# Performance work log

Measured on AMD Instinct MI355X. Metric: run time of the kernel, lower is better.

## Reference

```python
import jax, jax.numpy as jnp
import numpy as np

HS = 512   # hidden_size
IN = 2048  # input_size
MB = 100   # memory_bank_size
T  = 4096  # nImg


def setup_inputs() -> dict:
    key = jax.random.key(0)
    ks = jax.random.split(key, 20)

    def w(k, i, o):
        return jax.random.normal(k, (i, o), jnp.float32) * (1.0 / np.sqrt(i))

    def b(k, o):
        return jax.random.normal(k, (o,), jnp.float32) * 0.01

    return {
        "hidden_out_a": jax.random.normal(ks[0], (T, IN), jnp.float32),
        "hidden_out_m": jax.random.normal(ks[1], (T, IN), jnp.float32),
        "W_ca": w(ks[2], HS + IN, HS),  "b_ca": b(ks[3], HS),    # hidden_to_content_a
        "W_cm": w(ks[4], HS + IN, HS),  "b_cm": b(ks[5], HS),    # hidden_to_content_m
        "W_wp": w(ks[6], 3 * HS, 3),    "b_wp": b(ks[7], 3),     # write_prob
        "W_wpa": w(ks[8], HS + IN, MB), "b_wpa": b(ks[9], MB),   # write_prob_a
        "W_wpm": w(ks[10], HS + IN, MB),"b_wpm": b(ks[11], MB),  # write_prob_m
        "W_rp": w(ks[12], 3 * HS, MB),  "b_rp": b(ks[13], MB),   # read_prob
        "W_rh": w(ks[14], 2 * HS, HS),  "b_rh": b(ks[15], HS),   # read_to_hidden
        "W_rha": w(ks[16], 2 * HS + IN, HS), "b_rha": b(ks[17], HS),  # read_to_hidden_a
        "W_rhm": w(ks[18], 2 * HS + IN, HS), "b_rhm": b(ks[19], HS),  # read_to_hidden_m
        "nImg": T,
    }


def reference(hidden_out_a, hidden_out_m,
              W_ca, b_ca, W_cm, b_cm,
              W_wp, b_wp, W_wpa, b_wpa, W_wpm, b_wpm,
              W_rp, b_rp, W_rh, b_rh,
              W_rha, b_rha, W_rhm, b_rhm,
              nImg):
    hs = W_rh.shape[1]
    mb = W_rp.shape[1]

    def step(carry, xs):
        mem, h, ha, hm = carry            # mem: [MB, HS]; h/ha/hm: [HS]
        xa, xm = xs                       # [IN] each
        xh = jnp.concatenate([ha, hm, h])               # [3*HS]
        ar = jax.nn.softmax(xh @ W_rp + b_rp)           # [MB]
        r = ar @ mem                                    # [HS] memory read
        h1 = jax.nn.relu(jnp.concatenate([r, h]) @ W_rh + b_rh)
        ha1 = jax.nn.relu(jnp.concatenate([xa, r, ha]) @ W_rha + b_rha)
        hm1 = jax.nn.relu(jnp.concatenate([xm, r, hm]) @ W_rhm + b_rhm)
        aw = jax.nn.softmax(xh @ W_wp + b_wp)           # [3] stream gate
        xha = jnp.concatenate([ha, xa])                 # [HS+IN]
        xhm = jnp.concatenate([hm, xm])
        c_a = jax.nn.relu(xha @ W_ca + b_ca)            # [HS]
        c_m = jax.nn.relu(xhm @ W_cm + b_cm)
        aw_a = jax.nn.softmax(xha @ W_wpa + b_wpa)      # [MB]
        aw_m = jax.nn.softmax(xhm @ W_wpm + b_wpm)
        mem = aw[0] * mem + aw[1] * aw_a[:, None] * c_a + aw[2] * aw_m[:, None] * c_m
        return (mem, h1, ha1, hm1), h1

    init = (jnp.zeros((mb, hs), hidden_out_a.dtype),
            jnp.zeros((hs,), hidden_out_a.dtype),
            jnp.zeros((hs,), hidden_out_a.dtype),
            jnp.zeros((hs,), hidden_out_a.dtype))
    _, hiddens = jax.lax.scan(step, init,
                              (hidden_out_a[:nImg], hidden_out_m[:nImg]))
    return hiddens  # [nImg, HS]
```

## Files before the change

kernel.cpp:

```cpp
#include <hip/hip_runtime.h>
#include <cstdint>
#include <cstddef>

#define HS 512

constexpr int TPB  = 512;
constexpr int GBLK = 64;
constexpr int OWNB = 24;
constexpr int OWNW = 3;

constexpr size_t OFF_TWrp  = 0;
constexpr size_t OFF_TWwp  = OFF_TWrp  + 100*1536;
constexpr size_t OFF_TWwpa = OFF_TWwp  + 3*1536;
constexpr size_t OFF_TWwpm = OFF_TWwpa + 100*512;
constexpr size_t OFF_TWca  = OFF_TWwpm + 100*512;
constexpr size_t OFF_TWcm  = OFF_TWca  + 512*512;
constexpr size_t OFF_TWh0  = OFF_TWcm  + 512*512;
constexpr size_t OFF_TWh1  = OFF_TWh0  + 512*512;
constexpr size_t OFF_TWh2  = OFF_TWh1  + 512*512;
constexpr size_t OFF_TWu0  = OFF_TWh2  + 512*512;
constexpr size_t OFF_TWu1  = OFF_TWu0  + 512*512;
constexpr size_t OFF_TWu2  = OFF_TWu1  + 512*512;
constexpr size_t OFF_PAca  = OFF_TWu2  + 512*512;
constexpr size_t OFF_PMcm  = OFF_PAca  + 4096*512;
constexpr size_t OFF_PArha = OFF_PMcm  + 4096*512;
constexpr size_t OFF_PMrhm = OFF_PArha + 4096*512;
constexpr size_t OFF_PAwpa = OFF_PMrhm + 4096*512;
constexpr size_t OFF_PMwpm = OFF_PAwpa + 4096*100;
constexpr size_t OFF_CARRY = OFF_PMwpm + 4096*100;
constexpr size_t OFF_BCAST = OFF_CARRY + 2*1536*2;

__device__ __forceinline__ unsigned long long ald(const unsigned long long* p) {
  return __hip_atomic_load(const_cast<unsigned long long*>(p),
                           __ATOMIC_RELAXED, __HIP_MEMORY_SCOPE_AGENT);
}
__device__ __forceinline__ void gstTag(unsigned long long* p, float v, unsigned tag) {
  unsigned long long u = ((unsigned long long)tag << 32) | (unsigned long long)__float_as_uint(v);
  __hip_atomic_store(p, u, __ATOMIC_RELAXED, __HIP_MEMORY_SCOPE_AGENT);
}
__device__ __forceinline__ float xrsum(float v) {
  #pragma unroll
  for (int o = 32; o; o >>= 1) v += __shfl_xor(v, o, 64);
  return v;
}

template<int K4>
__device__ __forceinline__ float dotK(const float* __restrict__ w, const float* x) {
  int l = threadIdx.x & 63;
  const float4* w4 = (const float4*)w;
  const float4* x4 = (const float4*)x;
  float acc = 0.f;
  #pragma unroll
  for (int it = 0; it < K4; ++it) {
    float4 a = w4[l + 64*it];
    float4 b = x4[l + 64*it];
    acc += a.x*b.x + a.y*b.y + a.z*b.z + a.w*b.w;
  }
  return acc;
}

__device__ __forceinline__ void dot2K512(const float* __restrict__ w,
                                         const float* xa, const float* xm,
                                         float& ra, float& rm) {
  int l = threadIdx.x & 63;
  const float4* w4 = (const float4*)w;
  const float4* a4 = (const float4*)xa;
  const float4* m4 = (const float4*)xm;
  float sa = 0.f, sm = 0.f;
  #pragma unroll
  for (int it = 0; it < 2; ++it) {
    float4 wv = w4[l + 64*it], av = a4[l + 64*it], mv = m4[l + 64*it];
    sa += wv.x*av.x + wv.y*av.y + wv.z*av.z + wv.w*av.w;
    sm += wv.x*mv.x + wv.y*mv.y + wv.z*mv.z + wv.w*mv.w;
  }
  #pragma unroll
  for (int o = 32; o; o >>= 1) { sa += __shfl_xor(sa, o, 64); sm += __shfl_xor(sm, o, 64); }
  ra = sa; rm = sm;
}

__global__ void initK(unsigned long long* carryT, unsigned long long* bcast) {
  int i = blockIdx.x * blockDim.x + threadIdx.x, st = gridDim.x * blockDim.x;
  for (int k = i; k < 1536; k += st) carryT[k] = (1ull << 32);
  for (int k = i; k < 1536; k += st) carryT[1536 + k] = 0ull;
  for (int k = i; k < 2 * 1344; k += st) bcast[k] = 0ull;
}

__global__ void transK(const float* __restrict__ src, float* __restrict__ dst, int R, int C) {
  __shared__ float tile[32][33];
  int c0 = blockIdx.x * 32, r0 = blockIdx.y * 32;
  for (int i = threadIdx.y; i < 32; i += 8) {
    int r = r0 + i, c = c0 + threadIdx.x;
    tile[i][threadIdx.x] = (r < R && c < C) ? src[(size_t)r * C + c] : 0.f;
  }
  __syncthreads();
  for (int i = threadIdx.y; i < 32; i += 8) {
    int c = c0 + i, r = r0 + threadIdx.x;
    if (c < C && r < R) dst[(size_t)c * R + r] = tile[threadIdx.x][i];
  }
}

__global__ __launch_bounds__(256) void gemmK(const float* __restrict__ X,
                                             const float* __restrict__ W,
                                             float* __restrict__ C, int N) {
  __shared__ float As[16][68];
  __shared__ float Bs[16][68];
  int t0 = blockIdx.y * 64, n0 = blockIdx.x * 64;
  int tid = threadIdx.x, tx = tid & 15, ty = tid >> 4;
  float acc[4][4] = {};
  for (int k0 = 0; k0 < 2048; k0 += 16) {
    {
      int r = tid >> 2, c = (tid & 3) * 4;
      float4 v = *(const float4*)(X + (size_t)(t0 + r) * 2048 + k0 + c);
      As[c + 0][r] = v.x; As[c + 1][r] = v.y; As[c + 2][r] = v.z; As[c + 3][r] = v.w;
    }
    {
      int kr = tid >> 4, c = (tid & 15) * 4;
      int gcol = n0 + c;
      const float* src = W + (size_t)(k0 + kr) * N + gcol;
      #pragma unroll
      for (int i = 0; i < 4; ++i) Bs[kr][c + i] = (gcol + i < N) ? src[i] : 0.f;
    }
    __syncthreads();
    #pragma unroll
    for (int kk = 0; kk < 16; ++kk) {
      float4 a4 = *(const float4*)&As[kk][ty * 4];
      float4 b4 = *(const float4*)&Bs[kk][tx * 4];
      float av[4] = {a4.x, a4.y, a4.z, a4.w};
      float bv[4] = {b4.x, b4.y, b4.z, b4.w};
      #pragma unroll
      for (int i = 0; i < 4; ++i)
        #pragma unroll
        for (int j = 0; j < 4; ++j) acc[i][j] += av[i] * bv[j];
    }
    __syncthreads();
  }
  #pragma unroll
  for (int i = 0; i < 4; ++i)
    #pragma unroll
    for (int j = 0; j < 4; ++j) {
      int col = n0 + tx * 4 + j;
      if (col < N) C[(size_t)(t0 + ty * 4 + i) * N + col] = acc[i][j];
    }
}

__global__ __launch_bounds__(256) void gemm128(const float* __restrict__ X,
                                               const float* __restrict__ W,
                                               float* __restrict__ C) {
  __shared__ float As[8][132];
  __shared__ float Bs[8][132];
  const int N = 512;
  int t0 = blockIdx.y * 128, n0 = blockIdx.x * 128;
  int tid = threadIdx.x, tx = tid & 15, ty = tid >> 4;
  float acc[8][8] = {};
  for (int k0 = 0; k0 < 2048; k0 += 8) {
    int r = tid >> 1, c4 = (tid & 1) * 4;
    float4 va = *(const float4*)(X + (size_t)(t0 + r) * 2048 + k0 + c4);
    int kr = tid >> 5, cb = (tid & 31) * 4;
    float4 vb = *(const float4*)(W + (size_t)(k0 + kr) * N + n0 + cb);
    __syncthreads();
    As[c4 + 0][r] = va.x; As[c4 + 1][r] = va.y; As[c4 + 2][r] = va.z; As[c4 + 3][r] = va.w;
    Bs[kr][cb] = vb.x; Bs[kr][cb + 1] = vb.y; Bs[kr][cb + 2] = vb.z; Bs[kr][cb + 3] = vb.w;
    __syncthreads();
    #pragma unroll
    for (int kk = 0; kk < 8; ++kk) {
      float av[8], bv[8];
      *(float4*)av       = *(const float4*)&As[kk][ty * 8];
      *(float4*)(av + 4) = *(const float4*)&As[kk][ty * 8 + 4];
      *(float4*)bv       = *(const float4*)&Bs[kk][tx * 8];
      *(float4*)(bv + 4) = *(const float4*)&Bs[kk][tx * 8 + 4];
      #pragma unroll
      for (int i = 0; i < 8; ++i)
        #pragma unroll
        for (int j = 0; j < 8; ++j) acc[i][j] += av[i] * bv[j];
    }
  }
  #pragma unroll
  for (int i = 0; i < 8; ++i) {
    float* dst = C + (size_t)(t0 + ty * 8 + i) * N + n0 + tx * 8;
    *(float4*)dst       = *(float4*)&acc[i][0];
    *(float4*)(dst + 4) = *(float4*)&acc[i][4];
  }
}

struct RArgs {
  const float *TWrp, *TWwp, *TWwpa, *TWwpm, *TWca, *TWcm;
  const float *TWh0, *TWh1, *TWh2, *TWu0, *TWu1, *TWu2;
  const float *PAca, *PMcm, *PArha, *PMrhm, *PAwpa, *PMwpm;
  const float *b_ca, *b_cm, *b_wp, *b_wpa, *b_wpm, *b_rp, *b_rh, *b_rha, *b_rhm;
  unsigned long long *carryT, *bcast;
  float *out;
  int nT;
};

__global__ __launch_bounds__(TPB, 1) void recurK(RArgs a) {
  const int tid  = threadIdx.x;
  const int lane = tid & 63;
  const int lw   = tid >> 6;
  const int b    = blockIdx.x;

  __shared__ __align__(16) float s_wca[8 * 512];
  __shared__ __align__(16) float s_wcm[8 * 512];
  __shared__ __align__(16) float s_wbig[2 * 1536];
  __shared__ __align__(16) float s_wsm[4 * 512];
  __shared__ __align__(16) float s_TWu[OWNB * 512];
  __shared__ float s_G[OWNB * 104];
  __shared__ __align__(16) float s_x[1536];
  __shared__ __align__(16) float s_c[1024];
  __shared__ float s_ar[104], s_awa[104], s_awm[104], s_aw[4];
  __shared__ float s_part[OWNB];

  const int r0a = (b + 51) & 63;
  const int r1m = (b + 25) & 63;
  const bool big1_grp = (b < 36);
  const bool big1_wp  = (b >= 40 && b <= 42);

  for (int i = tid; i < 8 * 512; i += TPB) {
    int row = i >> 9, col = i & 511;
    s_wca[i] = a.TWca[(size_t)(b * 8 + row) * 512 + col];
    s_wcm[i] = a.TWcm[(size_t)(b * 8 + row) * 512 + col];
  }
  for (int i = tid; i < 1536; i += TPB) {
    s_wbig[i] = a.TWrp[(size_t)b * 1536 + i];
    float v2 = 0.f;
    if (big1_grp)      v2 = a.TWrp[(size_t)(b + 64) * 1536 + i];
    else if (big1_wp)  v2 = a.TWwp[(size_t)(b - 40) * 1536 + i];
    s_wbig[1536 + i] = v2;
  }
  for (int i = tid; i < 512; i += TPB) {
    s_wsm[i]        = a.TWwpa[(size_t)r0a * 512 + i];
    s_wsm[512 + i]  = (r0a < 36) ? a.TWwpa[(size_t)(r0a + 64) * 512 + i] : 0.f;
    s_wsm[1024 + i] = a.TWwpm[(size_t)r1m * 512 + i];
    s_wsm[1536 + i] = (r1m < 36) ? a.TWwpm[(size_t)(r1m + 64) * 512 + i] : 0.f;
  }
  for (int i = tid; i < OWNB * 512; i += TPB) {
    int rr = i >> 9, col = i & 511;
    int q = b * OWNB + rr, hsel = q >> 9, j = q & 511;
    const float* src = (hsel == 0) ? a.TWu0 : (hsel == 1) ? a.TWu1 : a.TWu2;
    s_TWu[i] = src[(size_t)j * 512 + col];
  }
  for (int i = tid; i < OWNB * 104; i += TPB) s_G[i] = 0.f;

  const int cacol = b * 8 + lw;
  const float bCa = a.b_ca[cacol];
  const float bCm = a.b_cm[cacol];

  int gtype = 0, gslot = 0, gdst = 0, gxoff = 0;
  const float* gpre = nullptr;
  float gbias = 0.f;
  if (lw == 7)      { gtype = 1; gslot = 0; gdst = 1024 + b; gbias = a.b_rp[b]; }
  else if (lw == 6) {
    if (big1_grp)     { gtype = 1; gslot = 1; gdst = 1024 + b + 64; gbias = a.b_rp[b + 64]; }
    else if (big1_wp) { gtype = 1; gslot = 1; gdst = 1324 + (b - 40); gbias = a.b_wp[b - 40]; }
  }
  else if (lw == 5) { gtype = 2; gslot = 0; gdst = 1124 + r0a; gxoff = 0;
                      gpre = a.PAwpa + r0a; gbias = a.b_wpa[r0a]; }
  else if (lw == 4 && r0a < 36) { gtype = 2; gslot = 1; gdst = 1124 + r0a + 64; gxoff = 0;
                      gpre = a.PAwpa + r0a + 64; gbias = a.b_wpa[r0a + 64]; }
  else if (lw == 3) { gtype = 2; gslot = 2; gdst = 1224 + r1m; gxoff = 512;
                      gpre = a.PMwpm + r1m; gbias = a.b_wpm[r1m]; }
  else if (lw == 2 && r1m < 36) { gtype = 2; gslot = 3; gdst = 1224 + r1m + 64; gxoff = 512;
                      gpre = a.PMwpm + r1m + 64; gbias = a.b_wpm[r1m + 64]; }

  int ownHsel[OWNW], ownJ[OWNW], whX[OWNW];
  float ownBias[OWNW];
  const float* ownPre[OWNW];
  const float* whRow[OWNW];
  #pragma unroll
  for (int k = 0; k < OWNW; ++k) {
    int q = b * OWNB + lw * OWNW + k, hsel = q >> 9, j = q & 511;
    ownHsel[k] = hsel; ownJ[k] = j;
    if (hsel == 0)      { ownBias[k] = a.b_rh[j];  ownPre[k] = nullptr;
                          whRow[k] = a.TWh0 + (size_t)j * 512; whX[k] = 1024; }
    else if (hsel == 1) { ownBias[k] = a.b_rha[j]; ownPre[k] = a.PArha + j;
                          whRow[k] = a.TWh1 + (size_t)j * 512; whX[k] = 0; }
    else                { ownBias[k] = a.b_rhm[j]; ownPre[k] = a.PMrhm + j;
                          whRow[k] = a.TWh2 + (size_t)j * 512; whX[k] = 512; }
  }
  __syncthreads();

  for (int t = 0; t < a.nT; ++t) {
    const unsigned tagB = (unsigned)t + 1;
    unsigned long long* bc = a.bcast + (size_t)(t & 1) * 1344;

    float preCa = a.PAca[(size_t)t * 512 + cacol];
    float preCm = a.PMcm[(size_t)t * 512 + cacol];
    float preG  = (gtype == 2) ? gpre[(size_t)t * 100] : 0.f;
    float preO[OWNW];
    #pragma unroll
    for (int k = 0; k < OWNW; ++k)
      preO[k] = ownPre[k] ? ownPre[k][(size_t)t * 512] : 0.f;

    {
      const unsigned long long* cin = a.carryT + (size_t)(t & 1) * 1536;
      int i0 = tid, i1 = tid + 512, i2 = tid + 1024;
      unsigned long long v0 = ald(cin + i0), v1 = ald(cin + i1), v2 = ald(cin + i2);
      while (((unsigned)(v0 >> 32) < tagB) | ((unsigned)(v1 >> 32) < tagB) |
             ((unsigned)(v2 >> 32) < tagB)) {
        __builtin_amdgcn_s_sleep(1);
        v0 = ald(cin + i0); v1 = ald(cin + i1); v2 = ald(cin + i2);
      }
      s_x[i0] = __uint_as_float((unsigned)v0);
      s_x[i1] = __uint_as_float((unsigned)v1);
      s_x[i2] = __uint_as_float((unsigned)v2);
    }
    __syncthreads();

    if (gtype == 1) {
      float v = xrsum(dotK<6>(s_wbig + gslot * 1536, s_x));
      if (!lane) gstTag(bc + gdst, v + gbias, tagB);
    } else if (gtype == 2) {
      float v = xrsum(dotK<2>(s_wsm + gslot * 512, s_x + gxoff));
      if (!lane) gstTag(bc + gdst, v + gbias + preG, tagB);
    }
    {
      float v = xrsum(dotK<2>(s_wca + lw * 512, s_x));
      if (!lane) gstTag(bc + cacol, fmaxf(v + preCa + bCa, 0.f), tagB);
      v = xrsum(dotK<2>(s_wcm + lw * 512, s_x + 512));
      if (!lane) gstTag(bc + 512 + cacol, fmaxf(v + preCm + bCm, 0.f), tagB);
    }
    #pragma unroll
    for (int k = 0; k < OWNW; ++k) {
      float v = xrsum(dotK<2>(whRow[k], s_x + whX[k]));
      if (!lane) s_part[lw * OWNW + k] = v;
    }

    if (lw < 3) {
      int base = 1024 + lw * 100;
      const unsigned long long* p1 = bc + base + lane;
      bool two = lane < 36;
      unsigned long long v1 = ald(p1);
      unsigned long long v2 = two ? ald(p1 + 64) : ~0ull;
      while (((unsigned)(v1 >> 32) < tagB) | ((unsigned)(v2 >> 32) < tagB)) {
        __builtin_amdgcn_s_sleep(1);
        v1 = ald(p1); if (two) v2 = ald(p1 + 64);
      }
      float x1 = __uint_as_float((unsigned)v1);
      float x2 = two ? __uint_as_float((unsigned)v2) : -3.0e38f;
      float m = fmaxf(x1, x2);
      #pragma unroll
      for (int o = 32; o; o >>= 1) m = fmaxf(m, __shfl_xor(m, o, 64));
      float e1 = expf(x1 - m);
      float e2 = two ? expf(x2 - m) : 0.f;
      float ss = e1 + e2;
      #pragma unroll
      for (int o = 32; o; o >>= 1) ss += __shfl_xor(ss, o, 64);
      float inv = 1.f / ss;
      float* dst = (lw == 0) ? s_ar : (lw == 1) ? s_awa : s_awm;
      dst[lane] = e1 * inv;
      if (two) dst[64 + lane] = e2 * inv;
    } else if (lw == 3) {
      float x = -3.0e38f;
      if (lane < 3) {
        const unsigned long long* p = bc + 1324 + lane;
        unsigned long long v = ald(p);
        while ((unsigned)(v >> 32) < tagB) { __builtin_amdgcn_s_sleep(1); v = ald(p); }
        x = __uint_as_float((unsigned)v);
      }
      float m = x;
      #pragma unroll
      for (int o = 32; o; o >>= 1) m = fmaxf(m, __shfl_xor(m, o, 64));
      float e = (lane < 3) ? expf(x - m) : 0.f;
      float ss = e;
      #pragma unroll
      for (int o = 32; o; o >>= 1) ss += __shfl_xor(ss, o, 64);
      if (lane < 3) s_aw[lane] = e / ss;
    } else {
      int base = tid - 256;
      const unsigned long long* p = bc + base;
      unsigned long long v0 = ald(p), v1 = ald(p + 256), v2 = ald(p + 512), v3 = ald(p + 768);
      while (((unsigned)(v0 >> 32) < tagB) | ((unsigned)(v1 >> 32) < tagB) |
             ((unsigned)(v2 >> 32) < tagB) | ((unsigned)(v3 >> 32) < tagB)) {
        __builtin_amdgcn_s_sleep(1);
        v0 = ald(p); v1 = ald(p + 256); v2 = ald(p + 512); v3 = ald(p + 768);
      }
      s_c[base]       = __uint_as_float((unsigned)v0);
      s_c[base + 256] = __uint_as_float((unsigned)v1);
      s_c[base + 512] = __uint_as_float((unsigned)v2);
      s_c[base + 768] = __uint_as_float((unsigned)v3);
    }
    __syncthreads();

    const float aw0 = s_aw[0], aw1 = s_aw[1], aw2 = s_aw[2];
    unsigned long long* cout = a.carryT + (size_t)((t + 1) & 1) * 1536;
    #pragma unroll
    for (int k = 0; k < OWNW; ++k) {
      int rr = lw * OWNW + k;
      float uA, uM;
      dot2K512(s_TWu + (size_t)rr * 512, s_c, s_c + 512, uA, uM);

      float* grow = s_G + rr * 104;
      bool two = lane < 36;
      float g1 = grow[lane];
      float g2 = two ? grow[64 + lane] : 0.f;
      float contrib = s_ar[lane] * g1 + (two ? s_ar[64 + lane] * g2 : 0.f);
      contrib = xrsum(contrib);
      grow[lane] = aw0 * g1 + aw1 * s_awa[lane] * uA + aw2 * s_awm[lane] * uM;
      if (two)
        grow[64 + lane] = aw0 * g2 + aw1 * s_awa[64 + lane] * uA + aw2 * s_awm[64 + lane] * uM;

      if (!lane) {
        int j = ownJ[k];
        float h = fmaxf(contrib + s_part[rr] + preO[k] + ownBias[k], 0.f);
        if (ownHsel[k] == 0) {
          a.out[(size_t)t * 512 + j] = h;
          gstTag(cout + 1024 + j, h, tagB + 1);
        } else if (ownHsel[k] == 1) {
          gstTag(cout + j, h, tagB + 1);
        } else {
          gstTag(cout + 512 + j, h, tagB + 1);
        }
      }
    }
    __syncthreads();
  }
}

extern "C" void kernel_launch(void* const* d_in, const int* in_sizes, int n_in,
                              void* d_out, int out_size, void* d_ws, size_t ws_size,
                              hipStream_t stream) {
  const float* Xa    = (const float*)d_in[0];
  const float* Xm    = (const float*)d_in[1];
  const float* W_ca  = (const float*)d_in[2];  const float* b_ca  = (const float*)d_in[3];
  const float* W_cm  = (const float*)d_in[4];  const float* b_cm  = (const float*)d_in[5];
  const float* W_wp  = (const float*)d_in[6];  const float* b_wp  = (const float*)d_in[7];
  const float* W_wpa = (const float*)d_in[8];  const float* b_wpa = (const float*)d_in[9];
  const float* W_wpm = (const float*)d_in[10]; const float* b_wpm = (const float*)d_in[11];
  const float* W_rp  = (const float*)d_in[12]; const float* b_rp  = (const float*)d_in[13];
  const float* W_rh  = (const float*)d_in[14]; const float* b_rh  = (const float*)d_in[15];
  const float* W_rha = (const float*)d_in[16]; const float* b_rha = (const float*)d_in[17];
  const float* W_rhm = (const float*)d_in[18]; const float* b_rhm = (const float*)d_in[19];

  int nT = out_size / HS;
  float* ws = (float*)d_ws;

  initK<<<dim3(64), dim3(256), 0, stream>>>(
      (unsigned long long*)(ws + OFF_CARRY),
      (unsigned long long*)(ws + OFF_BCAST));

  dim3 tb(32, 8);
  auto tg = [](int R, int C) { return dim3((C + 31) / 32, (R + 31) / 32); };
  transK<<<tg(1536, 100), tb, 0, stream>>>(W_rp,                       ws + OFF_TWrp,  1536, 100);
  transK<<<tg(1536, 3),   tb, 0, stream>>>(W_wp,                       ws + OFF_TWwp,  1536, 3);
  transK<<<tg(512, 100),  tb, 0, stream>>>(W_wpa,                      ws + OFF_TWwpa, 512, 100);
  transK<<<tg(512, 100),  tb, 0, stream>>>(W_wpm,                      ws + OFF_TWwpm, 512, 100);
  transK<<<tg(512, 512),  tb, 0, stream>>>(W_ca,                       ws + OFF_TWca,  512, 512);
  transK<<<tg(512, 512),  tb, 0, stream>>>(W_cm,                       ws + OFF_TWcm,  512, 512);
  transK<<<tg(512, 512),  tb, 0, stream>>>(W_rh  + 512 * 512,          ws + OFF_TWh0,  512, 512);
  transK<<<tg(512, 512),  tb, 0, stream>>>(W_rha + (size_t)2560 * 512, ws + OFF_TWh1,  512, 512);
  transK<<<tg(512, 512),  tb, 0, stream>>>(W_rhm + (size_t)2560 * 512, ws + OFF_TWh2,  512, 512);
  transK<<<tg(512, 512),  tb, 0, stream>>>(W_rh,                       ws + OFF_TWu0,  512, 512);
  transK<<<tg(512, 512),  tb, 0, stream>>>(W_rha + (size_t)2048 * 512, ws + OFF_TWu1,  512, 512);
  transK<<<tg(512, 512),  tb, 0, stream>>>(W_rhm + (size_t)2048 * 512, ws + OFF_TWu2,  512, 512);

  int tB = nT / 128;
  gemm128<<<dim3(4, tB), dim3(256), 0, stream>>>(Xa, W_ca + (size_t)512 * 512, ws + OFF_PAca);
  gemm128<<<dim3(4, tB), dim3(256), 0, stream>>>(Xm, W_cm + (size_t)512 * 512, ws + OFF_PMcm);
  gemm128<<<dim3(4, tB), dim3(256), 0, stream>>>(Xa, W_rha,                    ws + OFF_PArha);
  gemm128<<<dim3(4, tB), dim3(256), 0, stream>>>(Xm, W_rhm,                    ws + OFF_PMrhm);
  int tB64 = nT / 64;
  gemmK<<<dim3(2, tB64), dim3(256), 0, stream>>>(Xa, W_wpa + (size_t)512 * 100, ws + OFF_PAwpa, 100);
  gemmK<<<dim3(2, tB64), dim3(256), 0, stream>>>(Xm, W_wpm + (size_t)512 * 100, ws + OFF_PMwpm, 100);

  RArgs a;
  a.TWrp  = ws + OFF_TWrp;  a.TWwp  = ws + OFF_TWwp;
  a.TWwpa = ws + OFF_TWwpa; a.TWwpm = ws + OFF_TWwpm;
  a.TWca  = ws + OFF_TWca;  a.TWcm  = ws + OFF_TWcm;
  a.TWh0  = ws + OFF_TWh0;  a.TWh1  = ws + OFF_TWh1;  a.TWh2 = ws + OFF_TWh2;
  a.TWu0  = ws + OFF_TWu0;  a.TWu1  = ws + OFF_TWu1;  a.TWu2 = ws + OFF_TWu2;
  a.PAca  = ws + OFF_PAca;  a.PMcm  = ws + OFF_PMcm;
  a.PArha = ws + OFF_PArha; a.PMrhm = ws + OFF_PMrhm;
  a.PAwpa = ws + OFF_PAwpa; a.PMwpm = ws + OFF_PMwpm;
  a.b_ca = b_ca; a.b_cm = b_cm; a.b_wp = b_wp; a.b_wpa = b_wpa; a.b_wpm = b_wpm;
  a.b_rp = b_rp; a.b_rh = b_rh; a.b_rha = b_rha; a.b_rhm = b_rhm;
  a.carryT = (unsigned long long*)(ws + OFF_CARRY);
  a.bcast  = (unsigned long long*)(ws + OFF_BCAST);
  a.out    = (float*)d_out;
  a.nT     = nT;

  recurK<<<dim3(GBLK), dim3(TPB), 0, stream>>>(a);
}
```

Measured before the change: 28.08 ms.

## Remap recurrent dot products to 16-lane groups with padded LDS rows

Work inside the persistent recurrent kernel is redistributed from one 64-lane wavefront per row to 16-lane groups. Each group computes one content, gate or owned hidden row, with shorter shuffle reductions. Weight rows in LDS are padded to 516 floats and the G/softmax buffers to 112 entries to avoid bank conflicts. The trailing per-step __syncthreads and the s_part buffer are removed, and the hidden-row partial stays in a register. The aim is lower per-step latency on the serial critical path, at the cost of more per-lane loop iterations and reliance on the next step's barriers for correctness of s_G/s_c reuse.

After: 25.18 ms. 1.12x faster.

```diff
diff --git a/kernel.cpp b/kernel.cpp
--- a/kernel.cpp
+++ b/kernel.cpp
@@ -7,7 +7,7 @@
 constexpr int TPB  = 512;
 constexpr int GBLK = 64;
 constexpr int OWNB = 24;
-constexpr int OWNW = 3;
+constexpr int WPAD = 516;
 
 constexpr size_t OFF_TWrp  = 0;
 constexpr size_t OFF_TWwp  = OFF_TWrp  + 100*1536;
@@ -43,6 +43,11 @@
   for (int o = 32; o; o >>= 1) v += __shfl_xor(v, o, 64);
   return v;
 }
+__device__ __forceinline__ float rsum16(float v) {
+  #pragma unroll
+  for (int o = 8; o; o >>= 1) v += __shfl_xor(v, o, 64);
+  return v;
+}
 
 template<int K4>
 __device__ __forceinline__ float dotK(const float* __restrict__ w, const float* x) {
@@ -59,22 +64,35 @@
   return acc;
 }
 
-__device__ __forceinline__ void dot2K512(const float* __restrict__ w,
-                                         const float* xa, const float* xm,
-                                         float& ra, float& rm) {
-  int l = threadIdx.x & 63;
+__device__ __forceinline__ float dot16_512(const float* __restrict__ w,
+                                           const float* x, int gl) {
+  const float4* w4 = (const float4*)w;
+  const float4* x4 = (const float4*)x;
+  float acc = 0.f;
+  #pragma unroll
+  for (int it = 0; it < 8; ++it) {
+    float4 a = w4[gl + 16*it];
+    float4 b = x4[gl + 16*it];
+    acc += a.x*b.x + a.y*b.y + a.z*b.z + a.w*b.w;
+  }
+  return acc;
+}
+
+__device__ __forceinline__ void dot16_2x512(const float* __restrict__ w,
+                                            const float* xa, const float* xm,
+                                            int gl, float& ra, float& rm) {
   const float4* w4 = (const float4*)w;
   const float4* a4 = (const float4*)xa;
   const float4* m4 = (const float4*)xm;
   float sa = 0.f, sm = 0.f;
   #pragma unroll
-  for (int it = 0; it < 2; ++it) {
-    float4 wv = w4[l + 64*it], av = a4[l + 64*it], mv = m4[l + 64*it];
+  for (int it = 0; it < 8; ++it) {
+    float4 wv = w4[gl + 16*it], av = a4[gl + 16*it], mv = m4[gl + 16*it];
     sa += wv.x*av.x + wv.y*av.y + wv.z*av.z + wv.w*av.w;
     sm += wv.x*mv.x + wv.y*mv.y + wv.z*mv.z + wv.w*mv.w;
   }
   #pragma unroll
-  for (int o = 32; o; o >>= 1) { sa += __shfl_xor(sa, o, 64); sm += __shfl_xor(sm, o, 64); }
+  for (int o = 8; o; o >>= 1) { sa += __shfl_xor(sa, o, 64); sm += __shfl_xor(sm, o, 64); }
   ra = sa; rm = sm;
 }
 
@@ -196,28 +214,31 @@
   const int tid  = threadIdx.x;
   const int lane = tid & 63;
   const int lw   = tid >> 6;
+  const int g    = tid >> 4;
+  const int gl   = tid & 15;
   const int b    = blockIdx.x;
 
-  __shared__ __align__(16) float s_wca[8 * 512];
-  __shared__ __align__(16) float s_wcm[8 * 512];
+  __shared__ __align__(16) float s_wca[8 * WPAD];
+  __shared__ __align__(16) float s_wcm[8 * WPAD];
   __shared__ __align__(16) float s_wbig[2 * 1536];
-  __shared__ __align__(16) float s_wsm[4 * 512];
-  __shared__ __align__(16) float s_TWu[OWNB * 512];
-  __shared__ float s_G[OWNB * 104];
+  __shared__ __align__(16) float s_wsm[4 * WPAD];
+  __shared__ __align__(16) float s_TWu[OWNB * WPAD];
+  __shared__ __align__(16) float s_G[OWNB * 112];
   __shared__ __align__(16) float s_x[1536];
   __shared__ __align__(16) float s_c[1024];
-  __shared__ float s_ar[104], s_awa[104], s_awm[104], s_aw[4];
-  __shared__ float s_part[OWNB];
+  __shared__ float s_ar[112], s_awa[112], s_awm[112], s_aw[4];
 
   const int r0a = (b + 51) & 63;
   const int r1m = (b + 25) & 63;
   const bool big1_grp = (b < 36);
   const bool big1_wp  = (b >= 40 && b <= 42);
 
-  for (int i = tid; i < 8 * 512; i += TPB) {
-    int row = i >> 9, col = i & 511;
-    s_wca[i] = a.TWca[(size_t)(b * 8 + row) * 512 + col];
-    s_wcm[i] = a.TWcm[(size_t)(b * 8 + row) * 512 + col];
+  for (int i = tid; i < 8 * WPAD; i += TPB) {
+    int row = i / WPAD, col = i - row * WPAD;
+    if (col < 512) {
+      s_wca[i] = a.TWca[(size_t)(b * 8 + row) * 512 + col];
+      s_wcm[i] = a.TWcm[(size_t)(b * 8 + row) * 512 + col];
+    }
   }
   for (int i = tid; i < 1536; i += TPB) {
     s_wbig[i] = a.TWrp[(size_t)b * 1536 + i];
@@ -226,69 +247,71 @@
     else if (big1_wp)  v2 = a.TWwp[(size_t)(b - 40) * 1536 + i];
     s_wbig[1536 + i] = v2;
   }
-  for (int i = tid; i < 512; i += TPB) {
-    s_wsm[i]        = a.TWwpa[(size_t)r0a * 512 + i];
-    s_wsm[512 + i]  = (r0a < 36) ? a.TWwpa[(size_t)(r0a + 64) * 512 + i] : 0.f;
-    s_wsm[1024 + i] = a.TWwpm[(size_t)r1m * 512 + i];
-    s_wsm[1536 + i] = (r1m < 36) ? a.TWwpm[(size_t)(r1m + 64) * 512 + i] : 0.f;
-  }
-  for (int i = tid; i < OWNB * 512; i += TPB) {
-    int rr = i >> 9, col = i & 511;
-    int q = b * OWNB + rr, hsel = q >> 9, j = q & 511;
-    const float* src = (hsel == 0) ? a.TWu0 : (hsel == 1) ? a.TWu1 : a.TWu2;
-    s_TWu[i] = src[(size_t)j * 512 + col];
-  }
-  for (int i = tid; i < OWNB * 104; i += TPB) s_G[i] = 0.f;
-
-  const int cacol = b * 8 + lw;
-  const float bCa = a.b_ca[cacol];
-  const float bCm = a.b_cm[cacol];
-
-  int gtype = 0, gslot = 0, gdst = 0, gxoff = 0;
-  const float* gpre = nullptr;
-  float gbias = 0.f;
-  if (lw == 7)      { gtype = 1; gslot = 0; gdst = 1024 + b; gbias = a.b_rp[b]; }
-  else if (lw == 6) {
-    if (big1_grp)     { gtype = 1; gslot = 1; gdst = 1024 + b + 64; gbias = a.b_rp[b + 64]; }
-    else if (big1_wp) { gtype = 1; gslot = 1; gdst = 1324 + (b - 40); gbias = a.b_wp[b - 40]; }
-  }
-  else if (lw == 5) { gtype = 2; gslot = 0; gdst = 1124 + r0a; gxoff = 0;
-                      gpre = a.PAwpa + r0a; gbias = a.b_wpa[r0a]; }
-  else if (lw == 4 && r0a < 36) { gtype = 2; gslot = 1; gdst = 1124 + r0a + 64; gxoff = 0;
-                      gpre = a.PAwpa + r0a + 64; gbias = a.b_wpa[r0a + 64]; }
-  else if (lw == 3) { gtype = 2; gslot = 2; gdst = 1224 + r1m; gxoff = 512;
-                      gpre = a.PMwpm + r1m; gbias = a.b_wpm[r1m]; }
-  else if (lw == 2 && r1m < 36) { gtype = 2; gslot = 3; gdst = 1224 + r1m + 64; gxoff = 512;
-                      gpre = a.PMwpm + r1m + 64; gbias = a.b_wpm[r1m + 64]; }
-
-  int ownHsel[OWNW], ownJ[OWNW], whX[OWNW];
-  float ownBias[OWNW];
-  const float* ownPre[OWNW];
-  const float* whRow[OWNW];
-  #pragma unroll
-  for (int k = 0; k < OWNW; ++k) {
-    int q = b * OWNB + lw * OWNW + k, hsel = q >> 9, j = q & 511;
-    ownHsel[k] = hsel; ownJ[k] = j;
-    if (hsel == 0)      { ownBias[k] = a.b_rh[j];  ownPre[k] = nullptr;
-                          whRow[k] = a.TWh0 + (size_t)j * 512; whX[k] = 1024; }
-    else if (hsel == 1) { ownBias[k] = a.b_rha[j]; ownPre[k] = a.PArha + j;
-                          whRow[k] = a.TWh1 + (size_t)j * 512; whX[k] = 0; }
-    else                { ownBias[k] = a.b_rhm[j]; ownPre[k] = a.PMrhm + j;
-                          whRow[k] = a.TWh2 + (size_t)j * 512; whX[k] = 512; }
+  for (int i = tid; i < 4 * WPAD; i += TPB) {
+    int sl = i / WPAD, col = i - sl * WPAD;
+    float v = 0.f;
+    if (col < 512) {
+      if (sl == 0)      v = a.TWwpa[(size_t)r0a * 512 + col];
+      else if (sl == 1) v = (r0a < 36) ? a.TWwpa[(size_t)(r0a + 64) * 512 + col] : 0.f;
+      else if (sl == 2) v = a.TWwpm[(size_t)r1m * 512 + col];
+      else              v = (r1m < 36) ? a.TWwpm[(size_t)(r1m + 64) * 512 + col] : 0.f;
+    }
+    s_wsm[i] = v;
+  }
+  for (int i = tid; i < OWNB * WPAD; i += TPB) {
+    int rr = i / WPAD, col = i - rr * WPAD;
+    if (col < 512) {
+      int q = b * OWNB + rr, hsel = q >> 9, j = q & 511;
+      const float* src = (hsel == 0) ? a.TWu0 : (hsel == 1) ? a.TWu1 : a.TWu2;
+      s_TWu[i] = src[(size_t)j * 512 + col];
+    }
+  }
+  for (int i = tid; i < OWNB * 112; i += TPB) s_G[i] = 0.f;
+  if (tid < 112) { s_ar[tid] = 0.f; s_awa[tid] = 0.f; s_awm[tid] = 0.f; }
+
+  int dstA = -1, xoffA = 0, strideA = 512, rowA = 0;
+  float biasA = 0.f;
+  const float* preAPtr = nullptr;
+  if (lw < 2) {
+    int col = b * 8 + g; rowA = g;
+    dstA = col; biasA = a.b_ca[col]; preAPtr = a.PAca + col;
+  } else if (lw < 4) {
+    int col = b * 8 + (g - 8); rowA = g - 8;
+    dstA = 512 + col; biasA = a.b_cm[col]; preAPtr = a.PMcm + col;
+  } else if (lw == 4) {
+    int sl = g - 16;
+    if (sl == 0)                  { rowA = 0; dstA = 1124 + r0a;      biasA = a.b_wpa[r0a];      preAPtr = a.PAwpa + r0a;      xoffA = 0;   strideA = 100; }
+    else if (sl == 1 && r0a < 36) { rowA = 1; dstA = 1124 + r0a + 64; biasA = a.b_wpa[r0a + 64]; preAPtr = a.PAwpa + r0a + 64; xoffA = 0;   strideA = 100; }
+    else if (sl == 2)             { rowA = 2; dstA = 1224 + r1m;      biasA = a.b_wpm[r1m];      preAPtr = a.PMwpm + r1m;      xoffA = 512; strideA = 100; }
+    else if (sl == 3 && r1m < 36) { rowA = 3; dstA = 1224 + r1m + 64; biasA = a.b_wpm[r1m + 64]; preAPtr = a.PMwpm + r1m + 64; xoffA = 512; strideA = 100; }
+  }
+  int dstBig = -1, bigOff = 0;
+  float biasBig = 0.f;
+  if (lw == 6) { dstBig = 1024 + b; biasBig = a.b_rp[b]; bigOff = 0; }
+  else if (lw == 7) {
+    if (big1_grp)      { dstBig = 1024 + b + 64;  biasBig = a.b_rp[b + 64]; bigOff = 1536; }
+    else if (big1_wp)  { dstBig = 1324 + (b - 40); biasBig = a.b_wp[b - 40]; bigOff = 1536; }
+  }
+  int ownHsel = 0, ownJ = 0, whXo = 0;
+  float biasO = 0.f;
+  const float* preOPtr = nullptr;
+  const float* whPtr = nullptr;
+  if (g < OWNB) {
+    int q = b * OWNB + g, hsel = q >> 9, j = q & 511;
+    ownHsel = hsel; ownJ = j;
+    if (hsel == 0)      { biasO = a.b_rh[j];                           whPtr = a.TWh0 + (size_t)j * 512; whXo = 1024; }
+    else if (hsel == 1) { biasO = a.b_rha[j]; preOPtr = a.PArha + j;   whPtr = a.TWh1 + (size_t)j * 512; whXo = 0; }
+    else                { biasO = a.b_rhm[j]; preOPtr = a.PMrhm + j;   whPtr = a.TWh2 + (size_t)j * 512; whXo = 512; }
   }
   __syncthreads();
 
+  float whv = 0.f;
   for (int t = 0; t < a.nT; ++t) {
     const unsigned tagB = (unsigned)t + 1;
     unsigned long long* bc = a.bcast + (size_t)(t & 1) * 1344;
 
-    float preCa = a.PAca[(size_t)t * 512 + cacol];
-    float preCm = a.PMcm[(size_t)t * 512 + cacol];
-    float preG  = (gtype == 2) ? gpre[(size_t)t * 100] : 0.f;
-    float preO[OWNW];
-    #pragma unroll
-    for (int k = 0; k < OWNW; ++k)
-      preO[k] = ownPre[k] ? ownPre[k][(size_t)t * 512] : 0.f;
+    float preA = preAPtr ? preAPtr[(size_t)t * strideA] : 0.f;
+    float preO = preOPtr ? preOPtr[(size_t)t * 512] : 0.f;
 
     {
       const unsigned long long* cin = a.carryT + (size_t)(t & 1) * 1536;
@@ -305,24 +328,24 @@
     }
     __syncthreads();
 
-    if (gtype == 1) {
-      float v = xrsum(dotK<6>(s_wbig + gslot * 1536, s_x));
-      if (!lane) gstTag(bc + gdst, v + gbias, tagB);
-    } else if (gtype == 2) {
-      float v = xrsum(dotK<2>(s_wsm + gslot * 512, s_x + gxoff));
-      if (!lane) gstTag(bc + gdst, v + gbias + preG, tagB);
-    }
-    {
-      float v = xrsum(dotK<2>(s_wca + lw * 512, s_x));
-      if (!lane) gstTag(bc + cacol, fmaxf(v + preCa + bCa, 0.f), tagB);
-      v = xrsum(dotK<2>(s_wcm + lw * 512, s_x + 512));
-      if (!lane) gstTag(bc + 512 + cacol, fmaxf(v + preCm + bCm, 0.f), tagB);
-    }
-    #pragma unroll
-    for (int k = 0; k < OWNW; ++k) {
-      float v = xrsum(dotK<2>(whRow[k], s_x + whX[k]));
-      if (!lane) s_part[lw * OWNW + k] = v;
-    }
+    if (lw < 2) {
+      float v = rsum16(dot16_512(s_wca + rowA * WPAD, s_x, gl));
+      if (!gl) gstTag(bc + dstA, fmaxf(v + preA + biasA, 0.f), tagB);
+    } else if (lw < 4) {
+      float v = rsum16(dot16_512(s_wcm + rowA * WPAD, s_x + 512, gl));
+      if (!gl) gstTag(bc + dstA, fmaxf(v + preA + biasA, 0.f), tagB);
+    } else if (lw == 4) {
+      if (dstA >= 0) {
+        float v = rsum16(dot16_512(s_wsm + rowA * WPAD, s_x + xoffA, gl));
+        if (!gl) gstTag(bc + dstA, v + preA + biasA, tagB);
+      }
+    } else if (lw >= 6) {
+      if (dstBig >= 0) {
+        float v = xrsum(dotK<6>(s_wbig + bigOff, s_x));
+        if (!lane) gstTag(bc + dstBig, v + biasBig, tagB);
+      }
+    }
+    if (g < OWNB) whv = rsum16(dot16_512(whPtr, s_x + whXo, gl));
 
     if (lw < 3) {
       int base = 1024 + lw * 100;
@@ -380,38 +403,39 @@
     }
     __syncthreads();
 
-    const float aw0 = s_aw[0], aw1 = s_aw[1], aw2 = s_aw[2];
     unsigned long long* cout = a.carryT + (size_t)((t + 1) & 1) * 1536;
-    #pragma unroll
-    for (int k = 0; k < OWNW; ++k) {
-      int rr = lw * OWNW + k;
+    if (g < OWNB) {
+      const float aw0 = s_aw[0], aw1 = s_aw[1], aw2 = s_aw[2];
       float uA, uM;
-      dot2K512(s_TWu + (size_t)rr * 512, s_c, s_c + 512, uA, uM);
-
-      float* grow = s_G + rr * 104;
-      bool two = lane < 36;
-      float g1 = grow[lane];
-      float g2 = two ? grow[64 + lane] : 0.f;
-      float contrib = s_ar[lane] * g1 + (two ? s_ar[64 + lane] * g2 : 0.f);
-      contrib = xrsum(contrib);
-      grow[lane] = aw0 * g1 + aw1 * s_awa[lane] * uA + aw2 * s_awm[lane] * uM;
-      if (two)
-        grow[64 + lane] = aw0 * g2 + aw1 * s_awa[64 + lane] * uA + aw2 * s_awm[64 + lane] * uM;
-
-      if (!lane) {
-        int j = ownJ[k];
-        float h = fmaxf(contrib + s_part[rr] + preO[k] + ownBias[k], 0.f);
-        if (ownHsel[k] == 0) {
-          a.out[(size_t)t * 512 + j] = h;
-          gstTag(cout + 1024 + j, h, tagB + 1);
-        } else if (ownHsel[k] == 1) {
-          gstTag(cout + j, h, tagB + 1);
+      dot16_2x512(s_TWu + g * WPAD, s_c, s_c + 512, gl, uA, uM);
+
+      float* grow = s_G + g * 112;
+      float gv[7];
+      float contrib = 0.f;
+      #pragma unroll
+      for (int k = 0; k < 7; ++k) {
+        int idx = gl + 16 * k;
+        gv[k] = grow[idx];
+        contrib += s_ar[idx] * gv[k];
+      }
+      contrib = rsum16(contrib);
+      if (!gl) {
+        float h = fmaxf(contrib + whv + preO + biasO, 0.f);
+        if (ownHsel == 0) {
+          a.out[(size_t)t * 512 + ownJ] = h;
+          gstTag(cout + 1024 + ownJ, h, tagB + 1);
+        } else if (ownHsel == 1) {
+          gstTag(cout + ownJ, h, tagB + 1);
         } else {
-          gstTag(cout + 512 + j, h, tagB + 1);
+          gstTag(cout + 512 + ownJ, h, tagB + 1);
         }
       }
-    }
-    __syncthreads();
+      #pragma unroll
+      for (int k = 0; k < 7; ++k) {
+        int idx = gl + 16 * k;
+        grow[idx] = aw0 * gv[k] + aw1 * s_awa[idx] * uA + aw2 * s_awm[idx] * uM;
+      }
+    }
   }
 }
 
```
